# Kernel optimization log

Hardware: AMD Instinct MI355X
Metric: run time of the kernel (lower is better)

## Reference

```python
import jax, jax.numpy as jnp
import numpy as np

N_TASK = 100_000
N_DATA = 50_000
E = 1_500_000
D_TASK = 64
D_DATA = 64
D_EDGE = 16
H = 2
C = 64


def setup_inputs() -> dict:
    key = jax.random.key(0)
    ks = jax.random.split(key, 16)
    g = lambda k, shape, s=0.05: jax.random.normal(k, shape, jnp.float32) * s
    return {
        "task_x": jax.random.normal(ks[0], (N_TASK, D_TASK), jnp.float32),
        "data_x": jax.random.normal(ks[1], (N_DATA, D_DATA), jnp.float32),
        "edge_attr": jax.random.normal(ks[2], (E, D_EDGE), jnp.float32),
        "src_idx": jax.random.randint(ks[3], (E,), 0, N_DATA),
        "dst_idx": jax.random.randint(ks[4], (E,), 0, N_TASK),
        # GATv2Conv params
        "W_l": g(ks[5], (D_DATA, H * C)),   # lin_l (source/data)
        "b_l": jnp.zeros((H * C,), jnp.float32),
        "W_r": g(ks[6], (D_TASK, H * C)),   # lin_r (dest/tasks)
        "b_r": jnp.zeros((H * C,), jnp.float32),
        "W_e": g(ks[7], (D_EDGE, H * C)),   # lin_edge (no bias)
        "att": g(ks[8], (H, C)),
        "W_res": g(ks[9], (D_TASK, C)),     # residual lin (no bias)
        "conv_bias": jnp.zeros((C,), jnp.float32),
        # LayerNorm params
        "ln_g": jnp.ones((C,), jnp.float32),
        "ln_b": jnp.zeros((C,), jnp.float32),
    }


def reference(task_x, data_x, edge_attr, src_idx, dst_idx,
              W_l, b_l, W_r, b_r, W_e, att, W_res, conv_bias, ln_g, ln_b):
    n_task = task_x.shape[0]
    x_l = (data_x @ W_l + b_l).reshape(-1, H, C)      # [N_data, H, C]
    x_r = (task_x @ W_r + b_r).reshape(-1, H, C)      # [N_task, H, C]
    e = (edge_attr @ W_e).reshape(-1, H, C)           # [E, H, C]

    # GATv2 attention: leaky_relu(x_i + x_j + e) . att, negative_slope=0.2
    x = jax.nn.leaky_relu(x_l[src_idx] + x_r[dst_idx] + e, 0.2)  # [E, H, C]
    alpha = jnp.einsum("ehc,hc->eh", x, att)                      # [E, H]

    # per-destination-node segment softmax
    m = jax.ops.segment_max(alpha, dst_idx, num_segments=n_task)  # [N_task, H]
    m = jnp.where(jnp.isfinite(m), m, 0.0)  # empty segments -> 0
    a = jnp.exp(alpha - m[dst_idx])
    denom = jax.ops.segment_sum(a, dst_idx, num_segments=n_task)
    a = a / (denom[dst_idx] + 1e-16)                              # [E, H]

    # message = lin_l(x_src), weighted and scatter-summed to destinations
    out = jax.ops.segment_sum(x_l[src_idx] * a[..., None], dst_idx,
                              num_segments=n_task)                # [N_task, H, C]
    out = out.mean(axis=1)                                        # concat=False -> head mean
    out = out + task_x @ W_res + conv_bias                        # residual + bias

    # LayerNorm over channels
    mu = out.mean(-1, keepdims=True)
    var = out.var(-1, keepdims=True)
    out = (out - mu) / jnp.sqrt(var + 1e-5) * ln_g + ln_b

    out = jax.nn.leaky_relu(out, 0.01)
    return jnp.concatenate([out, task_x], axis=-1)                # [N_task, C + D_TASK]
```

## Files before the change

kernel.cpp:

```cpp
#include <hip/hip_runtime.h>
#include <hip/hip_bf16.h>

#define N_TASK 100000
#define N_DATA 50000
#define NE     1500000
#define PAD    48

typedef _Float16 half2v __attribute__((ext_vector_type(2)));
typedef float    f32x4  __attribute__((ext_vector_type(4)));
typedef unsigned u32x2  __attribute__((ext_vector_type(2)));
typedef int      i32x4  __attribute__((ext_vector_type(4)));

__device__ __forceinline__ unsigned pack_f16(float a, float b) {
    half2v h = {(_Float16)a, (_Float16)b};
    return __builtin_bit_cast(unsigned, h);
}
__device__ __forceinline__ float f16_lo(unsigned u) {
    half2v h = __builtin_bit_cast(half2v, u); return (float)h.x;
}
__device__ __forceinline__ float f16_hi(unsigned u) {
    half2v h = __builtin_bit_cast(half2v, u); return (float)h.y;
}
__device__ __forceinline__ float fdot2f(unsigned a, unsigned b, float c) {
#if __has_builtin(__builtin_amdgcn_fdot2)
    return __builtin_amdgcn_fdot2(__builtin_bit_cast(half2v, a),
                                  __builtin_bit_cast(half2v, b), c, false);
#else
    return c + f16_lo(a) * f16_lo(b) + f16_hi(a) * f16_hi(b);
#endif
}
__device__ __forceinline__ float fdot2h(half2v a, half2v b, float c) {
#if __has_builtin(__builtin_amdgcn_fdot2)
    return __builtin_amdgcn_fdot2(a, b, c, false);
#else
    return c + (float)a.x * (float)b.x + (float)a.y * (float)b.y;
#endif
}

template<int CTRL>
__device__ __forceinline__ float dppadd(float p) {
    int s = __builtin_amdgcn_update_dpp(0, __builtin_bit_cast(int, p),
                                        CTRL, 0xf, 0xf, false);
    return p + __builtin_bit_cast(float, s);
}
__device__ __forceinline__ float half_reduce(float p) {
    p = dppadd<0x121>(p);
    p = dppadd<0x122>(p);
    p = dppadd<0x124>(p);
    p = dppadd<0x128>(p);
    p += __builtin_bit_cast(float,
         __builtin_amdgcn_ds_swizzle(__builtin_bit_cast(int, p), 0x401F));
    return p;
}

__device__ __forceinline__ void gemm_tile64(
    const float* __restrict__ X, const float* __restrict__ W,
    const float* __restrict__ bias, unsigned* __restrict__ Yp,
    int nrows, int tb, float* Xs )
{
    int row0 = tb * 64;
    const float4* X4 = (const float4*)(X + (size_t)row0 * 64);
    float4* Xs4 = (float4*)Xs;
#pragma unroll
    for (int gi = 0; gi < 4; ++gi) {
        int g = threadIdx.x + gi * 256;
        float4 v = {0.f, 0.f, 0.f, 0.f};
        if (row0 + (g >> 4) < nrows) v = X4[g];
        Xs4[g] = v;
    }
    __syncthreads();
    int wv = threadIdx.x >> 6, lane = threadIdx.x & 63;
    const float* Xw = Xs + (wv * 16) * 64;
    float2 bb = *(const float2*)(bias + lane * 2);
    float2 acc[16];
#pragma unroll
    for (int r = 0; r < 16; ++r) acc[r] = bb;
#pragma unroll 4
    for (int k4 = 0; k4 < 16; ++k4) {
        float2 w0 = *(const float2*)(W + (k4 * 4 + 0) * 128 + lane * 2);
        float2 w1 = *(const float2*)(W + (k4 * 4 + 1) * 128 + lane * 2);
        float2 w2 = *(const float2*)(W + (k4 * 4 + 2) * 128 + lane * 2);
        float2 w3 = *(const float2*)(W + (k4 * 4 + 3) * 128 + lane * 2);
#pragma unroll
        for (int r = 0; r < 16; ++r) {
            float4 xv = *(const float4*)(Xw + r * 64 + k4 * 4);
            acc[r].x += xv.x * w0.x + xv.y * w1.x + xv.z * w2.x + xv.w * w3.x;
            acc[r].y += xv.x * w0.y + xv.y * w1.y + xv.z * w2.y + xv.w * w3.y;
        }
    }
#pragma unroll
    for (int r = 0; r < 16; ++r) {
        int row = row0 + wv * 16 + r;
        if (row < nrows)
            __builtin_nontemporal_store(pack_f16(acc[r].x, acc[r].y),
                                        &Yp[(size_t)row * 64 + lane]);
    }
}

__device__ __forceinline__ void gemm_tile64_res(
    const float* __restrict__ X, const float* __restrict__ W,
    const float* __restrict__ bias, unsigned short* __restrict__ Y16,
    int nrows, int tb, float* Xs)
{
    int row0 = tb * 64;
    const float4* X4 = (const float4*)(X + (size_t)row0 * 64);
    float4* Xs4 = (float4*)Xs;
#pragma unroll
    for (int gi = 0; gi < 4; ++gi) {
        int g = threadIdx.x + gi * 256;
        float4 v = {0.f, 0.f, 0.f, 0.f};
        if (row0 + (g >> 4) < nrows) v = X4[g];
        Xs4[g] = v;
    }
    __syncthreads();
    int wv = threadIdx.x >> 6, lane = threadIdx.x & 63;
    const float* Xw = Xs + (wv * 16) * 64;
    float bb = bias[lane];
    float acc[16];
#pragma unroll
    for (int r = 0; r < 16; ++r) acc[r] = bb;
#pragma unroll 4
    for (int k4 = 0; k4 < 16; ++k4) {
        float w0 = W[(k4 * 4 + 0) * 64 + lane];
        float w1 = W[(k4 * 4 + 1) * 64 + lane];
        float w2 = W[(k4 * 4 + 2) * 64 + lane];
        float w3 = W[(k4 * 4 + 3) * 64 + lane];
#pragma unroll
        for (int r = 0; r < 16; ++r) {
            float4 xv = *(const float4*)(Xw + r * 64 + k4 * 4);
            acc[r] += xv.x * w0 + xv.y * w1 + xv.z * w2 + xv.w * w3;
        }
    }
#pragma unroll
    for (int r = 0; r < 16; ++r) {
        int row = row0 + wv * 16 + r;
        if (row < nrows)
            __builtin_nontemporal_store(
                __builtin_bit_cast(unsigned short, (_Float16)acc[r]),
                &Y16[(size_t)row * 64 + lane]);
    }
}

#define FP_XR0   782
#define FP_RES0  2345
#define FP_WP    3908
#define FP_SC0   3909
#define SC_T     (1465 * 256)
__global__ __launch_bounds__(256) void fused_pre(
    const float* __restrict__ data_x, const float* __restrict__ Wl,
    const float* __restrict__ bl,
    const float* __restrict__ task_x, const float* __restrict__ Wr,
    const float* __restrict__ br,
    const float* __restrict__ Wres, const float* __restrict__ convb,
    const float* __restrict__ We,
    const float* __restrict__ ea, const int* __restrict__ dst,
    unsigned* __restrict__ xlb, unsigned* __restrict__ xrb,
    unsigned short* __restrict__ res16, u32x2* __restrict__ eafu2,
    unsigned* __restrict__ Wp, int* __restrict__ cnt,
    int* __restrict__ sedge)
{
    __shared__ float Xs[64 * 64];
    int b = blockIdx.x;
    if (b < FP_XR0) {
        gemm_tile64(data_x, Wl, bl, xlb, N_DATA, b, Xs);
    } else if (b < FP_RES0) {
        gemm_tile64(task_x, Wr, br, xrb, N_TASK, b - FP_XR0, Xs);
    } else if (b < FP_WP) {
        gemm_tile64_res(task_x, Wres, convb, res16, N_TASK, b - FP_RES0, Xs);
    } else if (b == FP_WP) {
#pragma unroll
        for (int r = 0; r < 4; ++r) {
            int idx = threadIdx.x * 4 + r;
            int kp = idx >> 7, col = idx & 127;
            Wp[idx] = pack_f16(We[(2 * kp) * 128 + col],
                               We[(2 * kp + 1) * 128 + col]);
        }
    } else {
        int g = (b - FP_SC0) * 256 + threadIdx.x;
#pragma unroll 4
        for (int h = 0; h < 16; ++h) {
            int idx = g + h * SC_T;
            if (idx < 6000000) {
                f32x4 q = __builtin_nontemporal_load((const f32x4*)ea + idx);
                u32x2 o;
                o.x = pack_f16(q.x, q.y);
                o.y = pack_f16(q.z, q.w);
                __builtin_nontemporal_store(o, eafu2 + idx);
            }
        }
        if (g < NE / 4) {
            i32x4 d = __builtin_nontemporal_load((const i32x4*)dst + g);
            int e = g * 4;
            int p0 = atomicAdd(&cnt[d.x], 1);
            if (p0 < PAD) __builtin_nontemporal_store(e,     &sedge[d.x * PAD + p0]);
            int p1 = atomicAdd(&cnt[d.y], 1);
            if (p1 < PAD) __builtin_nontemporal_store(e + 1, &sedge[d.y * PAD + p1]);
            int p2 = atomicAdd(&cnt[d.z], 1);
            if (p2 < PAD) __builtin_nontemporal_store(e + 2, &sedge[d.z * PAD + p2]);
            int p3 = atomicAdd(&cnt[d.w], 1);
            if (p3 < PAD) __builtin_nontemporal_store(e + 3, &sedge[d.w * PAD + p3]);
        }
    }
}

__global__ __launch_bounds__(256) void node_gat(
    const unsigned* __restrict__ xlb, const unsigned* __restrict__ xrb,
    const uint4* __restrict__ eaf, const unsigned* __restrict__ Wp,
    const float* __restrict__ att,
    const int* __restrict__ cntArr, const int* __restrict__ sedge,
    const int* __restrict__ src_idx,
    const unsigned short* __restrict__ res16, const float* __restrict__ tx,
    const float* __restrict__ g, const float* __restrict__ beta,
    float* __restrict__ out)
{
    int lane = threadIdx.x & 63;
    int li = lane & 31;
    int n = blockIdx.x * 4 + (threadIdx.x >> 6);
    if (n >= N_TASK) return;

    const uint2* Wp2 = (const uint2*)Wp;
    uint2 wp0 = Wp2[0 * 64 + lane], wp1 = Wp2[1 * 64 + lane];
    uint2 wp2 = Wp2[2 * 64 + lane], wp3 = Wp2[3 * 64 + lane];
    uint2 wp4 = Wp2[4 * 64 + lane], wp5 = Wp2[5 * 64 + lane];
    uint2 wp6 = Wp2[6 * 64 + lane], wp7 = Wp2[7 * 64 + lane];

    half2v xrh = __builtin_bit_cast(half2v, xrb[(unsigned)(n * 64 + lane)]);
    float2 atf = *(const float2*)(att + lane * 2);
    half2v ath = {(_Float16)(atf.x * 1.44269504f), (_Float16)(atf.y * 1.44269504f)};
    const half2v hpt2 = {(_Float16)0.2f, (_Float16)0.2f};

    int base = n * PAD;
    int cnt = __builtin_amdgcn_readfirstlane(cntArr[n]);
    cnt = cnt < PAD ? cnt : PAD;

    half2v acch = {(_Float16)0.f, (_Float16)0.f};
    float den = 0.f;

    auto palpha = [&](unsigned xu, uint4 u0, uint4 u1) -> float {
        float ev0 = 0.f, ev1 = 0.f;
        ev0 = fdot2f(u0.x, wp0.x, ev0); ev1 = fdot2f(u0.x, wp0.y, ev1);
        ev0 = fdot2f(u0.y, wp1.x, ev0); ev1 = fdot2f(u0.y, wp1.y, ev1);
        ev0 = fdot2f(u0.z, wp2.x, ev0); ev1 = fdot2f(u0.z, wp2.y, ev1);
        ev0 = fdot2f(u0.w, wp3.x, ev0); ev1 = fdot2f(u0.w, wp3.y, ev1);
        ev0 = fdot2f(u1.x, wp4.x, ev0); ev1 = fdot2f(u1.x, wp4.y, ev1);
        ev0 = fdot2f(u1.y, wp5.x, ev0); ev1 = fdot2f(u1.y, wp5.y, ev1);
        ev0 = fdot2f(u1.z, wp6.x, ev0); ev1 = fdot2f(u1.z, wp6.y, ev1);
        ev0 = fdot2f(u1.w, wp7.x, ev0); ev1 = fdot2f(u1.w, wp7.y, ev1);
        half2v z = __builtin_bit_cast(half2v, xu) + xrh
                 + __builtin_amdgcn_cvt_pkrtz(ev0, ev1);
        half2v z2 = z * hpt2;
#if __has_builtin(__builtin_elementwise_max)
        half2v lr = __builtin_elementwise_max(z, z2);
#else
        half2v lr; lr.x = z.x > z2.x ? z.x : z2.x; lr.y = z.y > z2.y ? z.y : z2.y;
#endif
        return fdot2h(lr, ath, 0.f);
    };
    auto accum = [&](float w, unsigned xu) {
        _Float16 wh = (_Float16)w;
        half2v w2 = {wh, wh};
        acch = acch + w2 * __builtin_bit_cast(half2v, xu);
        den += w;
    };

#define PAYLOAD(s_, e_, xu, e0, e1) do {                                     \
    xu = xlb[(unsigned)((s_) * 64 + lane)];                                  \
    const uint4* p_ = eaf + (unsigned)((e_) * 2);                            \
    e0 = p_[0]; e1 = p_[1];                                                  \
} while (0)

    int eidMA = 0, eidMB = 0, srcMA = 0, srcMB = 0;
    int eidFA = 0, eidFB = 0;
    unsigned xuA = 0, xuB = 0;
    uint4 A0 = {0,0,0,0}, A1 = {0,0,0,0}, B0 = {0,0,0,0}, B1 = {0,0,0,0};
    if (cnt > 0) {
        int e = __builtin_amdgcn_readfirstlane(sedge[base]);
        int s = __builtin_amdgcn_readfirstlane(src_idx[e]);
        PAYLOAD(s, e, xuA, A0, A1);
    }
    if (cnt > 1) {
        int e = __builtin_amdgcn_readfirstlane(sedge[base + 1]);
        int s = __builtin_amdgcn_readfirstlane(src_idx[e]);
        PAYLOAD(s, e, xuB, B0, B1);
    }
    if (cnt > 2) {
        eidMA = __builtin_amdgcn_readfirstlane(sedge[base + 2]);
        srcMA = __builtin_amdgcn_readfirstlane(src_idx[eidMA]);
    }
    if (cnt > 3) {
        eidMB = __builtin_amdgcn_readfirstlane(sedge[base + 3]);
        srcMB = __builtin_amdgcn_readfirstlane(src_idx[eidMB]);
    }
    if (cnt > 4) eidFA = sedge[base + 4];
    if (cnt > 5) eidFB = sedge[base + 5];

    int i = 0;
    for (; i + 2 <= cnt; i += 2) {
        float pA = palpha(xuA, A0, A1);
        float pB = palpha(xuB, B0, B1);
        unsigned cA = xuA, cB = xuB;
        if (i + 2 < cnt) PAYLOAD(srcMA, eidMA, xuA, A0, A1);
        if (i + 3 < cnt) PAYLOAD(srcMB, eidMB, xuB, B0, B1);
        if (i + 4 < cnt) {
            eidMA = __builtin_amdgcn_readfirstlane(eidFA);
            srcMA = __builtin_amdgcn_readfirstlane(src_idx[eidMA]);
        }
        if (i + 5 < cnt) {
            eidMB = __builtin_amdgcn_readfirstlane(eidFB);
            srcMB = __builtin_amdgcn_readfirstlane(src_idx[eidMB]);
        }
        if (i + 6 < cnt) eidFA = sedge[base + i + 6];
        if (i + 7 < cnt) eidFB = sedge[base + i + 7];
        pA = half_reduce(pA);
        pB = half_reduce(pB);
        accum(__builtin_amdgcn_exp2f(pA), cA);
        accum(__builtin_amdgcn_exp2f(pB), cB);
    }
    if (i < cnt) {
        float p = half_reduce(palpha(xuA, A0, A1));
        accum(__builtin_amdgcn_exp2f(p), xuA);
    }
#undef PAYLOAD

    float inv = 1.f / (den + 1e-16f);
    float o0 = (float)acch.x * inv, o1 = (float)acch.y * inv;

    float m0 = 0.5f * (o0 + __shfl_xor(o0, 32));
    float m1 = 0.5f * (o1 + __shfl_xor(o1, 32));

    unsigned ru = ((const unsigned*)res16)[(unsigned)(n * 32 + li)];
    float o0f = m0 + f16_lo(ru);
    float o1f = m1 + f16_hi(ru);

    float sum = o0f + o1f, ssq = o0f * o0f + o1f * o1f;
    sum = half_reduce(sum);
    ssq = half_reduce(ssq);
    float mu = sum * (1.f / 64.f);
    float var = ssq * (1.f / 64.f) - mu * mu;
    float is = rsqrtf(var + 1e-5f);
    float2 g2 = *(const float2*)(g + li * 2);
    float2 b2 = *(const float2*)(beta + li * 2);
    float x0o = (o0f - mu) * is * g2.x + b2.x;
    float x1o = (o1f - mu) * is * g2.y + b2.y;
    x0o = x0o > 0.f ? x0o : 0.01f * x0o;
    x1o = x1o > 0.f ? x1o : 0.01f * x1o;

    if (lane < 32) {
        float2 o = {x0o, x1o};
        *(float2*)(out + (size_t)n * 128 + li * 2) = o;
    } else {
        float2 t2 = *(const float2*)(tx + (size_t)n * 64 + li * 2);
        *(float2*)(out + (size_t)n * 128 + 64 + li * 2) = t2;
    }
}

extern "C" void kernel_launch(void* const* d_in, const int* in_sizes, int n_in,
                              void* d_out, int out_size, void* d_ws, size_t ws_size,
                              hipStream_t stream)
{
    const float* task_x    = (const float*)d_in[0];
    const float* data_x    = (const float*)d_in[1];
    const float* edge_attr = (const float*)d_in[2];
    const int*   src_idx   = (const int*)d_in[3];
    const int*   dst_idx   = (const int*)d_in[4];
    const float* W_l       = (const float*)d_in[5];
    const float* b_l       = (const float*)d_in[6];
    const float* W_r       = (const float*)d_in[7];
    const float* b_r       = (const float*)d_in[8];
    const float* W_e       = (const float*)d_in[9];
    const float* att       = (const float*)d_in[10];
    const float* W_res     = (const float*)d_in[11];
    const float* conv_bias = (const float*)d_in[12];
    const float* ln_g      = (const float*)d_in[13];
    const float* ln_b      = (const float*)d_in[14];
    float* out = (float*)d_out;

    unsigned* xlb   = (unsigned*)d_ws;
    unsigned* xrb   = xlb + 3200000;
    uint4*    eaf   = (uint4*)(xrb + 6400000);
    unsigned short* res16 = (unsigned short*)(eaf + 3000000);
    unsigned* Wp    = (unsigned*)(res16 + 6400000);
    int*      cnt   = (int*)(Wp + 1024);
    int*      sedge = cnt + 100000;

    (void)hipMemsetAsync(cnt, 0, 100000 * sizeof(int), stream);
    fused_pre<<<5374, 256, 0, stream>>>(data_x, W_l, b_l, task_x, W_r, b_r,
                                        W_res, conv_bias, W_e,
                                        edge_attr, dst_idx,
                                        xlb, xrb, res16, (u32x2*)eaf, Wp,
                                        cnt, sedge);
    node_gat <<<25000, 256, 0, stream>>>(xlb, xrb, eaf, Wp, att,
                                         cnt, sedge, src_idx,
                                         res16, task_x, ln_g, ln_b, out);
}
```

Before: 332.0 us.

## Drop edge_attr fp16 pre-pass and store (src,edge) pairs in bucket slots

Removes the pre-pass that converted all edge attributes to fp16. node_gat now reads the fp32 edge_attr rows directly and packs them to fp16 in registers. The bucketing step now writes the src index alongside the edge id, so node_gat no longer does a dependent src_idx lookup and its prefetch pipeline gets shallower. This removes a full read-and-write pass over edge_attr. In exchange the gather reads 64 bytes per edge instead of 32, and the sedge slots double in size.

```diff
diff --git a/kernel.cpp b/kernel.cpp
--- a/kernel.cpp
+++ b/kernel.cpp
@@ -8,7 +8,7 @@
 
 typedef _Float16 half2v __attribute__((ext_vector_type(2)));
 typedef float    f32x4  __attribute__((ext_vector_type(4)));
-typedef unsigned u32x2  __attribute__((ext_vector_type(2)));
+typedef int      i32x2  __attribute__((ext_vector_type(2)));
 typedef int      i32x4  __attribute__((ext_vector_type(4)));
 
 __device__ __forceinline__ unsigned pack_f16(float a, float b) {
@@ -20,6 +20,9 @@
 }
 __device__ __forceinline__ float f16_hi(unsigned u) {
     half2v h = __builtin_bit_cast(half2v, u); return (float)h.y;
+}
+__device__ __forceinline__ unsigned pkrtz(float a, float b) {
+    return __builtin_bit_cast(unsigned, __builtin_amdgcn_cvt_pkrtz(a, b));
 }
 __device__ __forceinline__ float fdot2f(unsigned a, unsigned b, float c) {
 #if __has_builtin(__builtin_amdgcn_fdot2)
@@ -145,7 +148,6 @@
 #define FP_RES0  2345
 #define FP_WP    3908
 #define FP_SC0   3909
-#define SC_T     (1465 * 256)
 __global__ __launch_bounds__(256) void fused_pre(
     const float* __restrict__ data_x, const float* __restrict__ Wl,
     const float* __restrict__ bl,
@@ -153,11 +155,11 @@
     const float* __restrict__ br,
     const float* __restrict__ Wres, const float* __restrict__ convb,
     const float* __restrict__ We,
-    const float* __restrict__ ea, const int* __restrict__ dst,
+    const int* __restrict__ src, const int* __restrict__ dst,
     unsigned* __restrict__ xlb, unsigned* __restrict__ xrb,
-    unsigned short* __restrict__ res16, u32x2* __restrict__ eafu2,
+    unsigned short* __restrict__ res16,
     unsigned* __restrict__ Wp, int* __restrict__ cnt,
-    int* __restrict__ sedge)
+    i32x2* __restrict__ sedge)
 {
     __shared__ float Xs[64 * 64];
     int b = blockIdx.x;
@@ -177,38 +179,31 @@
         }
     } else {
         int g = (b - FP_SC0) * 256 + threadIdx.x;
-#pragma unroll 4
-        for (int h = 0; h < 16; ++h) {
-            int idx = g + h * SC_T;
-            if (idx < 6000000) {
-                f32x4 q = __builtin_nontemporal_load((const f32x4*)ea + idx);
-                u32x2 o;
-                o.x = pack_f16(q.x, q.y);
-                o.y = pack_f16(q.z, q.w);
-                __builtin_nontemporal_store(o, eafu2 + idx);
-            }
-        }
         if (g < NE / 4) {
             i32x4 d = __builtin_nontemporal_load((const i32x4*)dst + g);
+            i32x4 s = __builtin_nontemporal_load((const i32x4*)src + g);
             int e = g * 4;
             int p0 = atomicAdd(&cnt[d.x], 1);
-            if (p0 < PAD) __builtin_nontemporal_store(e,     &sedge[d.x * PAD + p0]);
+            if (p0 < PAD) { i32x2 v = {s.x, e};
+                __builtin_nontemporal_store(v, &sedge[d.x * PAD + p0]); }
             int p1 = atomicAdd(&cnt[d.y], 1);
-            if (p1 < PAD) __builtin_nontemporal_store(e + 1, &sedge[d.y * PAD + p1]);
+            if (p1 < PAD) { i32x2 v = {s.y, e + 1};
+                __builtin_nontemporal_store(v, &sedge[d.y * PAD + p1]); }
             int p2 = atomicAdd(&cnt[d.z], 1);
-            if (p2 < PAD) __builtin_nontemporal_store(e + 2, &sedge[d.z * PAD + p2]);
+            if (p2 < PAD) { i32x2 v = {s.z, e + 2};
+                __builtin_nontemporal_store(v, &sedge[d.z * PAD + p2]); }
             int p3 = atomicAdd(&cnt[d.w], 1);
-            if (p3 < PAD) __builtin_nontemporal_store(e + 3, &sedge[d.w * PAD + p3]);
+            if (p3 < PAD) { i32x2 v = {s.w, e + 3};
+                __builtin_nontemporal_store(v, &sedge[d.w * PAD + p3]); }
         }
     }
 }
 
 __global__ __launch_bounds__(256) void node_gat(
     const unsigned* __restrict__ xlb, const unsigned* __restrict__ xrb,
-    const uint4* __restrict__ eaf, const unsigned* __restrict__ Wp,
+    const float* __restrict__ ea, const unsigned* __restrict__ Wp,
     const float* __restrict__ att,
-    const int* __restrict__ cntArr, const int* __restrict__ sedge,
-    const int* __restrict__ src_idx,
+    const int* __restrict__ cntArr, const i32x2* __restrict__ sedge,
     const unsigned short* __restrict__ res16, const float* __restrict__ tx,
     const float* __restrict__ g, const float* __restrict__ beta,
     float* __restrict__ out)
@@ -263,54 +258,37 @@
         den += w;
     };
 
-#define PAYLOAD(s_, e_, xu, e0, e1) do {                                     \
-    xu = xlb[(unsigned)((s_) * 64 + lane)];                                  \
-    const uint4* p_ = eaf + (unsigned)((e_) * 2);                            \
-    e0 = p_[0]; e1 = p_[1];                                                  \
+#define PAYLOAD(se, xu, e0, e1) do {                                         \
+    int s_ = __builtin_amdgcn_readfirstlane((se).x);                         \
+    int e_ = __builtin_amdgcn_readfirstlane((se).y);                         \
+    xu = xlb[(unsigned)(s_ * 64 + lane)];                                    \
+    const f32x4* p_ = (const f32x4*)(ea + (size_t)e_ * 16);                  \
+    f32x4 q0 = p_[0], q1 = p_[1], q2 = p_[2], q3 = p_[3];                    \
+    e0.x = pkrtz(q0.x, q0.y); e0.y = pkrtz(q0.z, q0.w);                      \
+    e0.z = pkrtz(q1.x, q1.y); e0.w = pkrtz(q1.z, q1.w);                      \
+    e1.x = pkrtz(q2.x, q2.y); e1.y = pkrtz(q2.z, q2.w);                      \
+    e1.z = pkrtz(q3.x, q3.y); e1.w = pkrtz(q3.z, q3.w);                      \
 } while (0)
 
-    int eidMA = 0, eidMB = 0, srcMA = 0, srcMB = 0;
-    int eidFA = 0, eidFB = 0;
+    i32x2 se0 = {0, 0}, se1 = {0, 0};
     unsigned xuA = 0, xuB = 0;
     uint4 A0 = {0,0,0,0}, A1 = {0,0,0,0}, B0 = {0,0,0,0}, B1 = {0,0,0,0};
-    if (cnt > 0) {
-        int e = __builtin_amdgcn_readfirstlane(sedge[base]);
-        int s = __builtin_amdgcn_readfirstlane(src_idx[e]);
-        PAYLOAD(s, e, xuA, A0, A1);
-    }
-    if (cnt > 1) {
-        int e = __builtin_amdgcn_readfirstlane(sedge[base + 1]);
-        int s = __builtin_amdgcn_readfirstlane(src_idx[e]);
-        PAYLOAD(s, e, xuB, B0, B1);
-    }
-    if (cnt > 2) {
-        eidMA = __builtin_amdgcn_readfirstlane(sedge[base + 2]);
-        srcMA = __builtin_amdgcn_readfirstlane(src_idx[eidMA]);
-    }
-    if (cnt > 3) {
-        eidMB = __builtin_amdgcn_readfirstlane(sedge[base + 3]);
-        srcMB = __builtin_amdgcn_readfirstlane(src_idx[eidMB]);
-    }
-    if (cnt > 4) eidFA = sedge[base + 4];
-    if (cnt > 5) eidFB = sedge[base + 5];
+    if (cnt > 0) se0 = sedge[base];
+    if (cnt > 1) se1 = sedge[base + 1];
+    if (cnt > 0) PAYLOAD(se0, xuA, A0, A1);
+    if (cnt > 1) PAYLOAD(se1, xuB, B0, B1);
+    if (cnt > 2) se0 = sedge[base + 2];
+    if (cnt > 3) se1 = sedge[base + 3];
 
     int i = 0;
     for (; i + 2 <= cnt; i += 2) {
         float pA = palpha(xuA, A0, A1);
         float pB = palpha(xuB, B0, B1);
         unsigned cA = xuA, cB = xuB;
-        if (i + 2 < cnt) PAYLOAD(srcMA, eidMA, xuA, A0, A1);
-        if (i + 3 < cnt) PAYLOAD(srcMB, eidMB, xuB, B0, B1);
-        if (i + 4 < cnt) {
-            eidMA = __builtin_amdgcn_readfirstlane(eidFA);
-            srcMA = __builtin_amdgcn_readfirstlane(src_idx[eidMA]);
-        }
-        if (i + 5 < cnt) {
-            eidMB = __builtin_amdgcn_readfirstlane(eidFB);
-            srcMB = __builtin_amdgcn_readfirstlane(src_idx[eidMB]);
-        }
-        if (i + 6 < cnt) eidFA = sedge[base + i + 6];
-        if (i + 7 < cnt) eidFB = sedge[base + i + 7];
+        if (i + 2 < cnt) PAYLOAD(se0, xuA, A0, A1);
+        if (i + 3 < cnt) PAYLOAD(se1, xuB, B0, B1);
+        if (i + 4 < cnt) se0 = sedge[base + i + 4];
+        if (i + 5 < cnt) se1 = sedge[base + i + 5];
         pA = half_reduce(pA);
         pB = half_reduce(pB);
         accum(__builtin_amdgcn_exp2f(pA), cA);
@@ -377,19 +355,17 @@
 
     unsigned* xlb   = (unsigned*)d_ws;
     unsigned* xrb   = xlb + 3200000;
-    uint4*    eaf   = (uint4*)(xrb + 6400000);
-    unsigned short* res16 = (unsigned short*)(eaf + 3000000);
+    unsigned short* res16 = (unsigned short*)(xrb + 6400000);
     unsigned* Wp    = (unsigned*)(res16 + 6400000);
     int*      cnt   = (int*)(Wp + 1024);
-    int*      sedge = cnt + 100000;
+    i32x2*    sedge = (i32x2*)(cnt + 100000);
 
     (void)hipMemsetAsync(cnt, 0, 100000 * sizeof(int), stream);
     fused_pre<<<5374, 256, 0, stream>>>(data_x, W_l, b_l, task_x, W_r, b_r,
                                         W_res, conv_bias, W_e,
-                                        edge_attr, dst_idx,
-                                        xlb, xrb, res16, (u32x2*)eaf, Wp,
-                                        cnt, sedge);
-    node_gat <<<25000, 256, 0, stream>>>(xlb, xrb, eaf, Wp, att,
-                                         cnt, sedge, src_idx,
+                                        src_idx, dst_idx,
+                                        xlb, xrb, res16, Wp, cnt, sedge);
+    node_gat <<<25000, 256, 0, stream>>>(xlb, xrb, edge_attr, Wp, att,
+                                         cnt, sedge,
                                          res16, task_x, ln_g, ln_b, out);
 }
```

Result: slower. 397.3 us (+19.7%).
